# Kernel optimization log

Hardware: AMD Instinct MI355X
Metric: run time of the kernel (lower is better)

The kernel has to match this reference:

```python
import jax, jax.numpy as jnp
import numpy as np
from jax.scipy.special import logsumexp

D = 1024      # d_model
H = 8         # num_heads
N = 16        # state_dim
ITERS = 5     # sinkhorn_iters
TAU = 1.0
B, S = 4, 1024
EPS = 1e-5


def setup_inputs() -> dict:
    key = jax.random.key(0)
    ks = jax.random.split(key, 8)
    x = jax.random.normal(ks[0], (B, S, D), dtype=jnp.float32)
    ln_w = jnp.ones((D,), jnp.float32)
    ln_b = jnp.zeros((D,), jnp.float32)
    # perm_proj: normal std=0.01, zero bias
    Wp = 0.01 * jax.random.normal(ks[1], (D, H * N * N), dtype=jnp.float32)
    bp = jnp.zeros((H * N * N,), jnp.float32)
    # gate_proj: normal std=0.01, bias=2.0
    Wg = 0.01 * jax.random.normal(ks[2], (D, H * N), dtype=jnp.float32)
    bg = jnp.full((H * N,), 2.0, jnp.float32)
    # input_proj / output_proj: xavier uniform, zero bias
    lim_i = float(np.sqrt(6.0 / (D + H * N)))
    Wi = jax.random.uniform(ks[3], (D, H * N), jnp.float32, -lim_i, lim_i)
    bi = jnp.zeros((H * N,), jnp.float32)
    Wo = jax.random.uniform(ks[4], (H * N, D), jnp.float32, -lim_i, lim_i)
    bo = jnp.zeros((D,), jnp.float32)
    return {"x": x, "ln_w": ln_w, "ln_b": ln_b, "Wp": Wp, "bp": bp,
            "Wg": Wg, "bg": bg, "Wi": Wi, "bi": bi, "Wo": Wo, "bo": bo}


def _sinkhorn(log_alpha):
    # log-space Sinkhorn: alternate row/column normalization
    for _ in range(ITERS):
        log_alpha = log_alpha - logsumexp(log_alpha, axis=-1, keepdims=True)
        log_alpha = log_alpha - logsumexp(log_alpha, axis=-2, keepdims=True)
    return jnp.exp(log_alpha)


def reference(x, ln_w, ln_b, Wp, bp, Wg, bg, Wi, bi, Wo, bo):
    residual = x
    # LayerNorm
    mu = jnp.mean(x, axis=-1, keepdims=True)
    var = jnp.var(x, axis=-1, keepdims=True)
    xn = (x - mu) * jax.lax.rsqrt(var + EPS) * ln_w + ln_b
    # projections
    logits = ((xn @ Wp + bp).reshape(B, S, H, N, N)) / TAU
    gamma = jax.nn.sigmoid((xn @ Wg + bg).reshape(B, S, H, N))
    b_in = (xn @ Wi + bi).reshape(B, S, H, N)
    # Sinkhorn for all timesteps at once (independent of recurrent state)
    soft = _sinkhorn(logits)                      # [B,S,H,N,N]
    # sequential state update over time
    Ps = jnp.moveaxis(soft, 1, 0)                 # [S,B,H,N,N]
    gs = jnp.moveaxis(gamma, 1, 0)                # [S,B,H,N]
    bs = jnp.moveaxis(b_in, 1, 0)                 # [S,B,H,N]

    def step(h, inp):
        P, g, b = inp
        h_perm = jnp.einsum('bhij,bhj->bhi', P, h)
        h_new = g * h_perm + (1.0 - g) * b
        return h_new, h_new

    h0 = jnp.zeros((B, H, N), x.dtype)
    _, hs = jax.lax.scan(step, h0, (Ps, gs, bs))  # hs: [S,B,H,N]
    out = jnp.moveaxis(hs, 0, 1).reshape(B, S, H * N)
    out = out @ Wo + bo                           # dropout = identity (eval)
    return residual + out
```

## Files before the change

kernel.cpp:

```cpp
#include <hip/hip_runtime.h>
#include <hip/hip_bf16.h>

#define D_    1024
#define H_    8
#define N_    16
#define B_    4
#define S_    1024
#define TOK   (B_*S_)
#define NPROJ 2304
#define CHUNK 32
#define NCHUNK (S_/CHUNK)
#define NCHAIN (B_*H_)

typedef __attribute__((ext_vector_type(8))) short bf16x8;
typedef __attribute__((ext_vector_type(4))) float f32x4;

typedef __attribute__((address_space(3))) void       as3_void;
typedef const __attribute__((address_space(1))) void as1_void;

__device__ __forceinline__ void gload_lds16(const void* g, void* l) {
    __builtin_amdgcn_global_load_lds((as1_void*)g, (as3_void*)l, 16, 0, 0);
}

__device__ __forceinline__ short f2bf(float f) {
    unsigned u = __builtin_bit_cast(unsigned, f);
    unsigned r = 0x7FFFu + ((u >> 16) & 1u);
    return (short)((u + r) >> 16);
}
__device__ __forceinline__ float bf2f(short s) {
    unsigned u = ((unsigned)(unsigned short)s) << 16;
    return __builtin_bit_cast(float, u);
}

template <int IMM>
__device__ __forceinline__ float swzf(float x) {
    return __builtin_bit_cast(float,
        __builtin_amdgcn_ds_swizzle(__builtin_bit_cast(int, x), IMM));
}
__device__ __forceinline__ float bpermf(int addr, float x) {
    return __builtin_bit_cast(float,
        __builtin_amdgcn_ds_bpermute(addr, __builtin_bit_cast(int, x)));
}
template <int CTRL>
__device__ __forceinline__ float dppmov(float x) {
    return __builtin_bit_cast(float,
        __builtin_amdgcn_update_dpp(0, __builtin_bit_cast(int, x),
                                    CTRL, 0xF, 0xF, true));
}
#define DPP_QX1  0xB1
#define DPP_QX2  0x4E
#define DPP_HMIR 0x141
#define DPP_ROR8 0x128

__global__ __launch_bounds__(256) void prep_kernel(const float* __restrict__ Wp,
                                                   const float* __restrict__ Wg,
                                                   const float* __restrict__ Wi,
                                                   const float* __restrict__ Wo,
                                                   short* __restrict__ WcatT,
                                                   short* __restrict__ WoT,
                                                   const float* __restrict__ x,
                                                   const float* __restrict__ lnw,
                                                   const float* __restrict__ lnb,
                                                   short* __restrict__ xn) {
    int id = blockIdx.x;
    if (id < 2432) {
        const float* src; short* dst; int srcW, Ksz, n_off, bx, by;
        if (id < 2048)      { src = Wp; dst = WcatT; srcW = 2048; Ksz = 1024; n_off = 0;
                              bx = id & 63;  by = id >> 6; }
        else if (id < 2176) { int q = id - 2048; src = Wg; dst = WcatT; srcW = 128; Ksz = 1024;
                              n_off = 2048; bx = q & 3; by = q >> 2; }
        else if (id < 2304) { int q = id - 2176; src = Wi; dst = WcatT; srcW = 128; Ksz = 1024;
                              n_off = 2176; bx = q & 3; by = q >> 2; }
        else                { int q = id - 2304; src = Wo; dst = WoT; srcW = 1024; Ksz = 128;
                              n_off = 0; bx = q & 31; by = q >> 5; }
        __shared__ float tile[32][33];
        int n0 = bx * 32, k0 = by * 32;
        int r  = threadIdx.x >> 3;
        int c4 = (threadIdx.x & 7) * 4;
        float4 v = *(const float4*)(src + (size_t)(k0 + r) * srcW + n0 + c4);
        tile[r][c4+0] = v.x; tile[r][c4+1] = v.y; tile[r][c4+2] = v.z; tile[r][c4+3] = v.w;
        __syncthreads();
        short4 o;
        o.x = f2bf(tile[c4+0][r]); o.y = f2bf(tile[c4+1][r]);
        o.z = f2bf(tile[c4+2][r]); o.w = f2bf(tile[c4+3][r]);
        *(short4*)(dst + (size_t)(n_off + n0 + r) * Ksz + k0 + c4) = o;
    } else {
        int row = id - 2432;
        int t = threadIdx.x;
        const float* xr = x + (size_t)row * D_;
        float4 v = *(const float4*)(xr + t * 4);
        float s  = v.x + v.y + v.z + v.w;
        float s2 = v.x*v.x + v.y*v.y + v.z*v.z + v.w*v.w;
        #pragma unroll
        for (int m = 1; m < 64; m <<= 1) { s += __shfl_xor(s, m); s2 += __shfl_xor(s2, m); }
        __shared__ float ps[4], ps2[4];
        if ((t & 63) == 0) { ps[t >> 6] = s; ps2[t >> 6] = s2; }
        __syncthreads();
        s  = ps[0] + ps[1] + ps[2] + ps[3];
        s2 = ps2[0] + ps2[1] + ps2[2] + ps2[3];
        float mu  = s * (1.0f / D_);
        float var = s2 * (1.0f / D_) - mu * mu;
        float inv = rsqrtf(var + 1e-5f);
        float4 wv = *(const float4*)(lnw + t * 4);
        float4 bv = *(const float4*)(lnb + t * 4);
        short4 o;
        o.x = f2bf((v.x - mu) * inv * wv.x + bv.x);
        o.y = f2bf((v.y - mu) * inv * wv.y + bv.y);
        o.z = f2bf((v.z - mu) * inv * wv.z + bv.z);
        o.w = f2bf((v.w - mu) * inv * wv.w + bv.w);
        *(short4*)(xn + (size_t)row * D_ + t * 4) = o;
    }
}

template <int MODE>
__global__ __launch_bounds__(512) void gemm_bt(const short* __restrict__ A,
                                               const short* __restrict__ BT,
                                               void* __restrict__ Cout,
                                               int M, int N, int K,
                                               const float* __restrict__ bias0,
                                               const float* __restrict__ bias1,
                                               const float* __restrict__ bias2,
                                               const float* __restrict__ resid) {
    __shared__ short lA[2][128 * 32];
    __shared__ short lB[2][128 * 32];
    const int nwg = gridDim.x;
    const int cpx = nwg >> 3;
    const int orig = blockIdx.x;
    const int wg = (orig & 7) * cpx + (orig >> 3);
    const int ntn = N >> 7;
    const int m0 = (wg / ntn) * 128, n0 = (wg % ntn) * 128;
    const int t = threadIdx.x, w = t >> 6, l = t & 63;
    const int wm = w >> 2, wn = w & 3;
    const int sr = l >> 2;
    const int sg = (l & 3) ^ ((l >> 3) & 3);
    const int fr = l & 15, fg = l >> 4;
    const int frag_off = fr * 32 + 8 * (fg ^ ((fr >> 1) & 3));

    f32x4 acc[4][2];
    #pragma unroll
    for (int mi = 0; mi < 4; ++mi)
        #pragma unroll
        for (int ni = 0; ni < 2; ++ni) acc[mi][ni] = (f32x4){0.f, 0.f, 0.f, 0.f};

    auto STAGE = [&](int bi, int k0) {
        int row = w * 16 + sr;
        gload_lds16(A  + (size_t)(m0 + row) * K + k0 + sg * 8, &lA[bi][w * 512]);
        gload_lds16(BT + (size_t)(n0 + row) * K + k0 + sg * 8, &lB[bi][w * 512]);
    };

    const int NT = K >> 5;
    STAGE(0, 0);
    if (NT > 1) STAGE(1, 32);
    asm volatile("s_waitcnt vmcnt(2)" ::: "memory");
    __builtin_amdgcn_s_barrier();

    int cur = 0;
    for (int kt = 0; kt < NT; ++kt) {
        bf16x8 af[4], bfr[2];
        #pragma unroll
        for (int mi = 0; mi < 4; ++mi)
            af[mi] = *(const bf16x8*)(&lA[cur][(wm * 4 + mi) * 512] + frag_off);
        #pragma unroll
        for (int ni = 0; ni < 2; ++ni)
            bfr[ni] = *(const bf16x8*)(&lB[cur][(wn * 2 + ni) * 512] + frag_off);
        asm volatile("s_waitcnt lgkmcnt(0)" ::: "memory");
        __builtin_amdgcn_sched_barrier(0);
        __builtin_amdgcn_s_barrier();
        if (kt + 2 < NT) STAGE(cur, (kt + 2) << 5);
        __builtin_amdgcn_s_setprio(1);
        #pragma unroll
        for (int mi = 0; mi < 4; ++mi)
            #pragma unroll
            for (int ni = 0; ni < 2; ++ni)
                acc[mi][ni] = __builtin_amdgcn_mfma_f32_16x16x32_bf16(af[mi], bfr[ni], acc[mi][ni], 0, 0, 0);
        __builtin_amdgcn_s_setprio(0);
        if (kt + 1 < NT) {
            if (kt + 2 < NT) asm volatile("s_waitcnt vmcnt(2)" ::: "memory");
            else             asm volatile("s_waitcnt vmcnt(0)" ::: "memory");
            __builtin_amdgcn_sched_barrier(0);
            __builtin_amdgcn_s_barrier();
        }
        cur ^= 1;
    }

    const int cr = (l >> 4) * 4, cc = l & 15;
    #pragma unroll
    for (int mi = 0; mi < 4; ++mi)
        #pragma unroll
        for (int ni = 0; ni < 2; ++ni) {
            int col = n0 + wn * 32 + ni * 16 + cc;
            float badd;
            if (MODE == 0)
                badd = (col < 2048) ? bias0[col] : (col < 2176 ? bias1[col - 2048] : bias2[col - 2176]);
            else
                badd = bias0[col];
            #pragma unroll
            for (int e = 0; e < 4; ++e) {
                int row = m0 + wm * 64 + mi * 16 + cr + e;
                float vout = acc[mi][ni][e] + badd;
                if (MODE == 0) {
                    ((short*)Cout)[(size_t)row * N + col] = f2bf(vout);
                } else {
                    vout += resid[(size_t)row * N + col];
                    ((float*)Cout)[(size_t)row * N + col] = vout;
                }
            }
        }
}

__global__ __launch_bounds__(256) void sinkhorn_kernel(const short* __restrict__ Cp,
                                                       short* __restrict__ Ahat,
                                                       float* __restrict__ u) {
    int w = threadIdx.x >> 6, l = threadIdx.x & 63;
    int id = blockIdx.x * 4 + w;
    int r = id >> 3, hh = id & 7;
    int a = l >> 3, b = l & 7;
    const short* base = Cp + (size_t)r * NPROJ + hh * 256;
    short2 q0 = *(const short2*)(base + (2 * a)     * 16 + 2 * b);
    short2 q1 = *(const short2*)(base + (2 * a + 1) * 16 + 2 * b);
    float p00 = __expf(bf2f(q0.x)), p01 = __expf(bf2f(q0.y));
    float p10 = __expf(bf2f(q1.x)), p11 = __expf(bf2f(q1.y));
    const int a32 = ((l ^ 32) << 2);
    #pragma unroll
    for (int it = 0; it < 5; ++it) {
        float r0 = p00 + p01, r1 = p10 + p11;
        r0 += dppmov<DPP_QX1>(r0);  r1 += dppmov<DPP_QX1>(r1);
        r0 += dppmov<DPP_QX2>(r0);  r1 += dppmov<DPP_QX2>(r1);
        r0 += dppmov<DPP_HMIR>(r0); r1 += dppmov<DPP_HMIR>(r1);
        float i0 = __builtin_amdgcn_rcpf(r0), i1 = __builtin_amdgcn_rcpf(r1);
        p00 *= i0; p01 *= i0; p10 *= i1; p11 *= i1;
        float c0 = p00 + p10, c1 = p01 + p11;
        c0 += dppmov<DPP_ROR8>(c0); c1 += dppmov<DPP_ROR8>(c1);
        c0 += swzf<0x401F>(c0);     c1 += swzf<0x401F>(c1);
        c0 += bpermf(a32, c0);      c1 += bpermf(a32, c1);
        float j0 = __builtin_amdgcn_rcpf(c0), j1 = __builtin_amdgcn_rcpf(c1);
        p00 *= j0; p10 *= j0; p01 *= j1; p11 *= j1;
    }
    short2 gp = *(const short2*)(Cp + (size_t)r * NPROJ + 2048 + hh * 16 + 2 * a);
    short2 bn = *(const short2*)(Cp + (size_t)r * NPROJ + 2176 + hh * 16 + 2 * a);
    float g0 = 1.f / (1.f + __expf(-bf2f(gp.x)));
    float g1 = 1.f / (1.f + __expf(-bf2f(gp.y)));
    short2 o0, o1;
    o0.x = f2bf(g0 * p00); o0.y = f2bf(g0 * p01);
    o1.x = f2bf(g1 * p10); o1.y = f2bf(g1 * p11);
    short* Ao = Ahat + (size_t)id * 256;
    *(short2*)(Ao + (2 * a)     * 16 + 2 * b) = o0;
    *(short2*)(Ao + (2 * a + 1) * 16 + 2 * b) = o1;
    if (b == 0) {
        float2 uo;
        uo.x = (1.f - g0) * bf2f(bn.x);
        uo.y = (1.f - g1) * bf2f(bn.y);
        *(float2*)(u + (size_t)id * 16 + 2 * a) = uo;
    }
}

__global__ __launch_bounds__(64) void pass1_kernel(const short* __restrict__ Ahat,
                                                   const float* __restrict__ u,
                                                   float* __restrict__ Mc,
                                                   float* __restrict__ vc) {
    __shared__ short lAh[CHUNK * 256];
    __shared__ float lu[CHUNK * 16];
    int unit = blockIdx.x;
    int chain = unit >> 5, c = unit & 31;
    int b = chain >> 3, hh = chain & 7;
    int l = threadIdx.x;
    int j = l & 15, g = l >> 4;
    const size_t id0 = ((size_t)(b * S_ + c * CHUNK)) * H_ + hh;

    #pragma unroll
    for (int q = 0; q < 16; ++q) {
        int m = q * 2 + (l >> 5);
        gload_lds16(Ahat + (id0 + (size_t)m * H_) * 256 + (l & 31) * 8,
                    (char*)lAh + q * 1024);
    }
    #pragma unroll
    for (int q = 0; q < 2; ++q) {
        int sl = q * 16 + (l >> 2);
        gload_lds16(u + (id0 + (size_t)sl * H_) * 16 + (l & 3) * 4,
                    (char*)lu + q * 1024);
    }
    asm volatile("s_waitcnt vmcnt(0)" ::: "memory");

    bf16x8 mb = {0,0,0,0,0,0,0,0};
    bf16x8 vb = {0,0,0,0,0,0,0,0};
    #pragma unroll
    for (int e = 0; e < 4; ++e) if (4 * g + e == j) mb[e] = (short)0x3F80;
    const f32x4 zero = {0.f, 0.f, 0.f, 0.f};
    f32x4 d = zero, dv = zero;
    #pragma unroll 4
    for (int tt = 0; tt < CHUNK; ++tt) {
        short4 pa = *(const short4*)(&lAh[tt * 256 + j * 16 + g * 4]);
        bf16x8 af = {0,0,0,0,0,0,0,0};
        af[0] = pa.x; af[1] = pa.y; af[2] = pa.z; af[3] = pa.w;
        d  = __builtin_amdgcn_mfma_f32_16x16x32_bf16(af, mb, zero, 0, 0, 0);
        dv = __builtin_amdgcn_mfma_f32_16x16x32_bf16(af, vb, zero, 0, 0, 0);
        if (j == 0) {
            dv[0] += lu[tt * 16 + 4 * g + 0];
            dv[1] += lu[tt * 16 + 4 * g + 1];
            dv[2] += lu[tt * 16 + 4 * g + 2];
            dv[3] += lu[tt * 16 + 4 * g + 3];
        }
        mb[0] = f2bf(d[0]);  mb[1] = f2bf(d[1]);  mb[2] = f2bf(d[2]);  mb[3] = f2bf(d[3]);
        vb[0] = f2bf(dv[0]); vb[1] = f2bf(dv[1]); vb[2] = f2bf(dv[2]); vb[3] = f2bf(dv[3]);
    }
    float* Mo = Mc + (size_t)unit * 256;
    #pragma unroll
    for (int e = 0; e < 4; ++e) Mo[(4 * g + e) * 16 + j] = d[e];
    if (j == 0) {
        #pragma unroll
        for (int e = 0; e < 4; ++e) vc[(size_t)unit * 16 + 4 * g + e] = dv[e];
    }
}

__global__ __launch_bounds__(64) void pass2_kernel(const float* __restrict__ Mc,
                                                   const float* __restrict__ vc,
                                                   float* __restrict__ hstart) {
    int chain = blockIdx.x;
    int l = threadIdx.x, i = l & 15;
    float h = 0.f;
    size_t u0 = (size_t)chain * NCHUNK;
    const float* Mr = Mc + u0 * 256 + i * 16;
    float4 m0 = *(const float4*)(Mr);
    float4 m1 = *(const float4*)(Mr + 4);
    float4 m2 = *(const float4*)(Mr + 8);
    float4 m3 = *(const float4*)(Mr + 12);
    float vcur = vc[u0 * 16 + i];
    for (int c = 0; c < NCHUNK; ++c) {
        size_t unit = u0 + c;
        if (l < 16) hstart[unit * 16 + i] = h;
        float4 n0 = m0, n1 = m1, n2 = m2, n3 = m3;
        float vnext = vcur;
        if (c + 1 < NCHUNK) {
            const float* Mn = Mc + (unit + 1) * 256 + i * 16;
            n0 = *(const float4*)(Mn);
            n1 = *(const float4*)(Mn + 4);
            n2 = *(const float4*)(Mn + 8);
            n3 = *(const float4*)(Mn + 12);
            vnext = vc[(unit + 1) * 16 + i];
        }
        float acc = vcur;
        acc += m0.x * __shfl(h, 0)  + m0.y * __shfl(h, 1)  + m0.z * __shfl(h, 2)  + m0.w * __shfl(h, 3);
        acc += m1.x * __shfl(h, 4)  + m1.y * __shfl(h, 5)  + m1.z * __shfl(h, 6)  + m1.w * __shfl(h, 7);
        acc += m2.x * __shfl(h, 8)  + m2.y * __shfl(h, 9)  + m2.z * __shfl(h, 10) + m2.w * __shfl(h, 11);
        acc += m3.x * __shfl(h, 12) + m3.y * __shfl(h, 13) + m3.z * __shfl(h, 14) + m3.w * __shfl(h, 15);
        h = acc;
        m0 = n0; m1 = n1; m2 = n2; m3 = n3; vcur = vnext;
    }
}

__global__ __launch_bounds__(64) void pass3_kernel(const short* __restrict__ Ahat,
                                                   const float* __restrict__ u,
                                                   const float* __restrict__ hstart,
                                                   short* __restrict__ hs) {
    __shared__ short lAh[CHUNK * 256];
    __shared__ float lu[CHUNK * 16];
    int unit = blockIdx.x;
    int chain = unit >> 5, c = unit & 31;
    int b = chain >> 3, hh = chain & 7;
    int l = threadIdx.x, i = l & 15, g = l >> 4;
    const size_t id0 = ((size_t)(b * S_ + c * CHUNK)) * H_ + hh;

    #pragma unroll
    for (int q = 0; q < 16; ++q) {
        int m = q * 2 + (l >> 5);
        gload_lds16(Ahat + (id0 + (size_t)m * H_) * 256 + (l & 31) * 8,
                    (char*)lAh + q * 1024);
    }
    #pragma unroll
    for (int q = 0; q < 2; ++q) {
        int sl = q * 16 + (l >> 2);
        gload_lds16(u + (id0 + (size_t)sl * H_) * 16 + (l & 3) * 4,
                    (char*)lu + q * 1024);
    }
    float4 h0 = *(const float4*)(hstart + (size_t)unit * 16 + g * 4);
    float h_0 = h0.x, h_1 = h0.y, h_2 = h0.z, h_3 = h0.w;
    asm volatile("s_waitcnt vmcnt(0)" ::: "memory");

    #pragma unroll 4
    for (int tt = 0; tt < CHUNK; ++tt) {
        size_t r = (size_t)b * S_ + c * CHUNK + tt;
        short4 pa = *(const short4*)(&lAh[tt * 256 + i * 16 + g * 4]);
        float part = bf2f(pa.x) * h_0 + bf2f(pa.y) * h_1 + bf2f(pa.z) * h_2 + bf2f(pa.w) * h_3;
        part += __shfl_xor(part, 16);
        part += __shfl_xor(part, 32);
        float hnew = part + lu[tt * 16 + i];
        if (g == 0) hs[r * 128 + hh * 16 + i] = f2bf(hnew);
        h_0 = __shfl(hnew, 4 * g + 0);
        h_1 = __shfl(hnew, 4 * g + 1);
        h_2 = __shfl(hnew, 4 * g + 2);
        h_3 = __shfl(hnew, 4 * g + 3);
    }
}

extern "C" void kernel_launch(void* const* d_in, const int* in_sizes, int n_in,
                              void* d_out, int out_size, void* d_ws, size_t ws_size,
                              hipStream_t stream) {
    const float* x    = (const float*)d_in[0];
    const float* ln_w = (const float*)d_in[1];
    const float* ln_b = (const float*)d_in[2];
    const float* Wp   = (const float*)d_in[3];
    const float* bp   = (const float*)d_in[4];
    const float* Wg   = (const float*)d_in[5];
    const float* bg   = (const float*)d_in[6];
    const float* Wi   = (const float*)d_in[7];
    const float* bi   = (const float*)d_in[8];
    const float* Wo   = (const float*)d_in[9];
    const float* bo   = (const float*)d_in[10];
    float* out = (float*)d_out;

    char* ws = (char*)d_ws;
    constexpr size_t OFF_WCATT = 0;
    constexpr size_t OFF_WOT   = OFF_WCATT + (size_t)NPROJ * D_ * 2;
    constexpr size_t OFF_XN    = OFF_WOT   + (size_t)D_ * 128 * 2;
    constexpr size_t OFF_CP    = OFF_XN    + (size_t)TOK * D_ * 2;
    constexpr size_t OFF_AHAT  = OFF_CP    + (size_t)TOK * NPROJ * 2;
    constexpr size_t OFF_U     = OFF_AHAT  + (size_t)TOK * H_ * 256 * 2;
    constexpr size_t OFF_MC    = OFF_U     + (size_t)TOK * H_ * 16 * 4;
    constexpr size_t OFF_VC    = OFF_MC    + (size_t)NCHAIN * NCHUNK * 256 * 4;
    constexpr size_t OFF_HST   = OFF_VC    + (size_t)NCHAIN * NCHUNK * 16 * 4;
    constexpr size_t OFF_HS    = OFF_HST   + (size_t)NCHAIN * NCHUNK * 16 * 4;

    short* WcatT = (short*)(ws + OFF_WCATT);
    short* WoT   = (short*)(ws + OFF_WOT);
    short* xn    = (short*)(ws + OFF_XN);
    short* Cp    = (short*)(ws + OFF_CP);
    short* Ahat  = (short*)(ws + OFF_AHAT);
    float* u     = (float*)(ws + OFF_U);
    float* Mc    = (float*)(ws + OFF_MC);
    float* vc    = (float*)(ws + OFF_VC);
    float* hst   = (float*)(ws + OFF_HST);
    short* hs    = (short*)(ws + OFF_HS);

    prep_kernel<<<2432 + TOK, 256, 0, stream>>>(Wp, Wg, Wi, Wo, WcatT, WoT,
                                                x, ln_w, ln_b, xn);
    gemm_bt<0><<<(NPROJ / 128) * (TOK / 128), 512, 0, stream>>>(
        xn, WcatT, (void*)Cp, TOK, NPROJ, 1024, bp, bg, bi, nullptr);
    sinkhorn_kernel<<<(TOK * H_) / 4, 256, 0, stream>>>(Cp, Ahat, u);
    pass1_kernel<<<NCHAIN * NCHUNK, 64, 0, stream>>>(Ahat, u, Mc, vc);
    pass2_kernel<<<NCHAIN, 64, 0, stream>>>(Mc, vc, hst);
    pass3_kernel<<<NCHAIN * NCHUNK, 64, 0, stream>>>(Ahat, u, hst, hs);
    gemm_bt<1><<<(D_ / 128) * (TOK / 128), 512, 0, stream>>>(
        hs, WoT, (void*)out, TOK, D_, 128, bo, nullptr, nullptr, x);
}
```

Measured before the change: 100.9 us.

## Fuse chunk-carry scan into pass3 by redundantly replaying prefix chunks per block

```diff
diff --git a/kernel.cpp b/kernel.cpp
--- a/kernel.cpp
+++ b/kernel.cpp
@@ -256,7 +256,7 @@
 
 __global__ __launch_bounds__(64) void pass1_kernel(const short* __restrict__ Ahat,
                                                    const float* __restrict__ u,
-                                                   float* __restrict__ Mc,
+                                                   short* __restrict__ Mc,
                                                    float* __restrict__ vc) {
     __shared__ short lAh[CHUNK * 256];
     __shared__ float lu[CHUNK * 16];
@@ -303,57 +303,22 @@
         mb[0] = f2bf(d[0]);  mb[1] = f2bf(d[1]);  mb[2] = f2bf(d[2]);  mb[3] = f2bf(d[3]);
         vb[0] = f2bf(dv[0]); vb[1] = f2bf(dv[1]); vb[2] = f2bf(dv[2]); vb[3] = f2bf(dv[3]);
     }
-    float* Mo = Mc + (size_t)unit * 256;
-    #pragma unroll
-    for (int e = 0; e < 4; ++e) Mo[(4 * g + e) * 16 + j] = d[e];
+    short* Mo = Mc + (size_t)unit * 256;
+    #pragma unroll
+    for (int e = 0; e < 4; ++e) Mo[(4 * g + e) * 16 + j] = mb[e];
     if (j == 0) {
         #pragma unroll
         for (int e = 0; e < 4; ++e) vc[(size_t)unit * 16 + 4 * g + e] = dv[e];
     }
 }
 
-__global__ __launch_bounds__(64) void pass2_kernel(const float* __restrict__ Mc,
-                                                   const float* __restrict__ vc,
-                                                   float* __restrict__ hstart) {
-    int chain = blockIdx.x;
-    int l = threadIdx.x, i = l & 15;
-    float h = 0.f;
-    size_t u0 = (size_t)chain * NCHUNK;
-    const float* Mr = Mc + u0 * 256 + i * 16;
-    float4 m0 = *(const float4*)(Mr);
-    float4 m1 = *(const float4*)(Mr + 4);
-    float4 m2 = *(const float4*)(Mr + 8);
-    float4 m3 = *(const float4*)(Mr + 12);
-    float vcur = vc[u0 * 16 + i];
-    for (int c = 0; c < NCHUNK; ++c) {
-        size_t unit = u0 + c;
-        if (l < 16) hstart[unit * 16 + i] = h;
-        float4 n0 = m0, n1 = m1, n2 = m2, n3 = m3;
-        float vnext = vcur;
-        if (c + 1 < NCHUNK) {
-            const float* Mn = Mc + (unit + 1) * 256 + i * 16;
-            n0 = *(const float4*)(Mn);
-            n1 = *(const float4*)(Mn + 4);
-            n2 = *(const float4*)(Mn + 8);
-            n3 = *(const float4*)(Mn + 12);
-            vnext = vc[(unit + 1) * 16 + i];
-        }
-        float acc = vcur;
-        acc += m0.x * __shfl(h, 0)  + m0.y * __shfl(h, 1)  + m0.z * __shfl(h, 2)  + m0.w * __shfl(h, 3);
-        acc += m1.x * __shfl(h, 4)  + m1.y * __shfl(h, 5)  + m1.z * __shfl(h, 6)  + m1.w * __shfl(h, 7);
-        acc += m2.x * __shfl(h, 8)  + m2.y * __shfl(h, 9)  + m2.z * __shfl(h, 10) + m2.w * __shfl(h, 11);
-        acc += m3.x * __shfl(h, 12) + m3.y * __shfl(h, 13) + m3.z * __shfl(h, 14) + m3.w * __shfl(h, 15);
-        h = acc;
-        m0 = n0; m1 = n1; m2 = n2; m3 = n3; vcur = vnext;
-    }
-}
-
-__global__ __launch_bounds__(64) void pass3_kernel(const short* __restrict__ Ahat,
-                                                   const float* __restrict__ u,
-                                                   const float* __restrict__ hstart,
-                                                   short* __restrict__ hs) {
-    __shared__ short lAh[CHUNK * 256];
-    __shared__ float lu[CHUNK * 16];
+__global__ __launch_bounds__(64) void pass23_kernel(const short* __restrict__ Ahat,
+                                                    const float* __restrict__ u,
+                                                    const short* __restrict__ Mc,
+                                                    const float* __restrict__ vc,
+                                                    short* __restrict__ hs) {
+    __shared__ short mats[64 * 256];
+    __shared__ float vecs[64 * 16];
     int unit = blockIdx.x;
     int chain = unit >> 5, c = unit & 31;
     int b = chain >> 3, hh = chain & 7;
@@ -364,26 +329,45 @@
     for (int q = 0; q < 16; ++q) {
         int m = q * 2 + (l >> 5);
         gload_lds16(Ahat + (id0 + (size_t)m * H_) * 256 + (l & 31) * 8,
-                    (char*)lAh + q * 1024);
+                    (char*)mats + q * 1024);
     }
     #pragma unroll
     for (int q = 0; q < 2; ++q) {
         int sl = q * 16 + (l >> 2);
         gload_lds16(u + (id0 + (size_t)sl * H_) * 16 + (l & 3) * 4,
-                    (char*)lu + q * 1024);
-    }
-    float4 h0 = *(const float4*)(hstart + (size_t)unit * 16 + g * 4);
-    float h_0 = h0.x, h_1 = h0.y, h_2 = h0.z, h_3 = h0.w;
+                    (char*)vecs + q * 1024);
+    }
+    const short* McB = Mc + (size_t)chain * NCHUNK * 256;
+    const int nmc = (c + 1) >> 1;
+    for (int q = 0; q < nmc; ++q)
+        gload_lds16(McB + q * 512 + l * 8, (char*)mats + 16384 + q * 1024);
+    const float* vcB = vc + (size_t)chain * NCHUNK * 16;
+    const int nvc = (c + 15) >> 4;
+    for (int q = 0; q < nvc; ++q)
+        gload_lds16(vcB + q * 256 + l * 4, (char*)vecs + 2048 + q * 1024);
+
     asm volatile("s_waitcnt vmcnt(0)" ::: "memory");
 
+    float h_0 = 0.f, h_1 = 0.f, h_2 = 0.f, h_3 = 0.f;
+    for (int cc = 0; cc < c; ++cc) {
+        short4 pa = *(const short4*)(&mats[(32 + cc) * 256 + i * 16 + g * 4]);
+        float part = bf2f(pa.x) * h_0 + bf2f(pa.y) * h_1 + bf2f(pa.z) * h_2 + bf2f(pa.w) * h_3;
+        part += __shfl_xor(part, 16);
+        part += __shfl_xor(part, 32);
+        float hnew = part + vecs[(32 + cc) * 16 + i];
+        h_0 = __shfl(hnew, 4 * g + 0);
+        h_1 = __shfl(hnew, 4 * g + 1);
+        h_2 = __shfl(hnew, 4 * g + 2);
+        h_3 = __shfl(hnew, 4 * g + 3);
+    }
     #pragma unroll 4
     for (int tt = 0; tt < CHUNK; ++tt) {
         size_t r = (size_t)b * S_ + c * CHUNK + tt;
-        short4 pa = *(const short4*)(&lAh[tt * 256 + i * 16 + g * 4]);
+        short4 pa = *(const short4*)(&mats[tt * 256 + i * 16 + g * 4]);
         float part = bf2f(pa.x) * h_0 + bf2f(pa.y) * h_1 + bf2f(pa.z) * h_2 + bf2f(pa.w) * h_3;
         part += __shfl_xor(part, 16);
         part += __shfl_xor(part, 32);
-        float hnew = part + lu[tt * 16 + i];
+        float hnew = part + vecs[tt * 16 + i];
         if (g == 0) hs[r * 128 + hh * 16 + i] = f2bf(hnew);
         h_0 = __shfl(hnew, 4 * g + 0);
         h_1 = __shfl(hnew, 4 * g + 1);
@@ -416,9 +400,8 @@
     constexpr size_t OFF_AHAT  = OFF_CP    + (size_t)TOK * NPROJ * 2;
     constexpr size_t OFF_U     = OFF_AHAT  + (size_t)TOK * H_ * 256 * 2;
     constexpr size_t OFF_MC    = OFF_U     + (size_t)TOK * H_ * 16 * 4;
-    constexpr size_t OFF_VC    = OFF_MC    + (size_t)NCHAIN * NCHUNK * 256 * 4;
-    constexpr size_t OFF_HST   = OFF_VC    + (size_t)NCHAIN * NCHUNK * 16 * 4;
-    constexpr size_t OFF_HS    = OFF_HST   + (size_t)NCHAIN * NCHUNK * 16 * 4;
+    constexpr size_t OFF_VC    = OFF_MC    + (size_t)NCHAIN * NCHUNK * 256 * 2;
+    constexpr size_t OFF_HS    = OFF_VC    + (size_t)NCHAIN * NCHUNK * 16 * 4;
 
     short* WcatT = (short*)(ws + OFF_WCATT);
     short* WoT   = (short*)(ws + OFF_WOT);
@@ -426,9 +409,8 @@
     short* Cp    = (short*)(ws + OFF_CP);
     short* Ahat  = (short*)(ws + OFF_AHAT);
     float* u     = (float*)(ws + OFF_U);
-    float* Mc    = (float*)(ws + OFF_MC);
+    short* Mc    = (short*)(ws + OFF_MC);
     float* vc    = (float*)(ws + OFF_VC);
-    float* hst   = (float*)(ws + OFF_HST);
     short* hs    = (short*)(ws + OFF_HS);
 
     prep_kernel<<<2432 + TOK, 256, 0, stream>>>(Wp, Wg, Wi, Wo, WcatT, WoT,
@@ -437,8 +419,7 @@
         xn, WcatT, (void*)Cp, TOK, NPROJ, 1024, bp, bg, bi, nullptr);
     sinkhorn_kernel<<<(TOK * H_) / 4, 256, 0, stream>>>(Cp, Ahat, u);
     pass1_kernel<<<NCHAIN * NCHUNK, 64, 0, stream>>>(Ahat, u, Mc, vc);
-    pass2_kernel<<<NCHAIN, 64, 0, stream>>>(Mc, vc, hst);
-    pass3_kernel<<<NCHAIN * NCHUNK, 64, 0, stream>>>(Ahat, u, hst, hs);
+    pass23_kernel<<<NCHAIN * NCHUNK, 64, 0, stream>>>(Ahat, u, Mc, vc, hs);
     gemm_bt<1><<<(D_ / 128) * (TOK / 128), 512, 0, stream>>>(
         hs, WoT, (void*)out, TOK, D_, 128, bo, nullptr, nullptr, x);
 }
```

Result: faster. 92.22 us (-8.6%).
